# Optimization experiments

Hardware: AMD Instinct MI355X
Metric: run time of the kernel (lower is better)

## Reference

```python
import jax, jax.numpy as jnp
import numpy as np

B, C, H, W = 16, 512, 32, 32
CI = C // 2
EPS = 1e-5


def _lin_params(k, din, dout):
    kw, kb = jax.random.split(k)
    w = jax.random.normal(kw, (dout, din), jnp.float32) * (1.0 / np.sqrt(din))
    b = jax.random.normal(kb, (dout,), jnp.float32) * 0.01
    return w, b


def _bn_params(k):
    k1, k2, k3, k4 = jax.random.split(k, 4)
    g = 1.0 + 0.05 * jax.random.normal(k1, (C,), jnp.float32)
    b = 0.05 * jax.random.normal(k2, (C,), jnp.float32)
    m = 0.1 * jax.random.normal(k3, (C,), jnp.float32)
    v = jax.random.uniform(k4, (C,), jnp.float32, 0.5, 1.5)
    return g, b, m, v


def setup_inputs() -> dict:
    key = jax.random.key(0)
    ks = jax.random.split(key, 12)
    inp = {
        'rgb_cm': jax.random.normal(ks[0], (B, C, H, W), jnp.float32),
        'flow_cm': jax.random.normal(ks[1], (B, C, H, W), jnp.float32),
    }
    for i, pfx in enumerate(['1', '2']):
        g, b, m, v = _bn_params(ks[2 + 5 * i])
        inp[f'bn{pfx}_g'], inp[f'bn{pfx}_b'] = g, b
        inp[f'bn{pfx}_m'], inp[f'bn{pfx}_v'] = m, v
        inp[f'th{pfx}_w'], inp[f'th{pfx}_b'] = _lin_params(ks[3 + 5 * i], C, CI)
        inp[f'ph{pfx}_w'], inp[f'ph{pfx}_b'] = _lin_params(ks[4 + 5 * i], C, CI)
        inp[f'g{pfx}_w'], inp[f'g{pfx}_b'] = _lin_params(ks[5 + 5 * i], C, CI)
        inp[f'w{pfx}_w'], inp[f'w{pfx}_b'] = _lin_params(ks[6 + 5 * i], CI, C)
    return inp


def _bn_relu(x, g, b, m, v):
    # x: [B, C, num]; eval-mode BatchNorm1d over channel dim, then ReLU
    scale = (g * jax.lax.rsqrt(v + EPS))[None, :, None]
    shift = (b - m * g * jax.lax.rsqrt(v + EPS))[None, :, None]
    return jax.nn.relu(x * scale + shift)


def _can(A, Bx, bn_g, bn_b, bn_m, bn_v, th_w, th_b, ph_w, ph_b, g_w, g_b, w_w, w_b):
    # A, Bx: [B, C, num]
    A = _bn_relu(A, bn_g, bn_b, bn_m, bn_v).transpose(0, 2, 1)   # [B, num, C]
    Bx = _bn_relu(Bx, bn_g, bn_b, bn_m, bn_v).transpose(0, 2, 1)  # [B, num, C]
    x_theta = A @ th_w.T + th_b      # [B, num, CI]
    x_phi = Bx @ ph_w.T + ph_b       # [B, num, CI]
    attn = jnp.einsum('bnc,bmc->bnm', x_theta, x_phi)  # [B, num, num] (unscaled)
    f_div_C = jax.nn.softmax(attn, axis=-1)
    g_x = A @ g_w.T + g_b            # [B, num, CI]
    y = jnp.einsum('bnm,bmc->bnc', f_div_C, g_x)
    W_y = y @ w_w.T + w_b            # [B, num, C]
    return (A + W_y).transpose(0, 2, 1)  # [B, C, num]


def reference(rgb_cm, flow_cm,
              bn1_g, bn1_b, bn1_m, bn1_v, th1_w, th1_b, ph1_w, ph1_b, g1_w, g1_b, w1_w, w1_b,
              bn2_g, bn2_b, bn2_m, bn2_v, th2_w, th2_b, ph2_w, ph2_b, g2_w, g2_b, w2_w, w2_b):
    b, c, h, w = rgb_cm.shape
    rgb_f = rgb_cm.reshape(b, c, h * w)
    flow_f = flow_cm.reshape(b, c, h * w)
    att_rgb = _can(rgb_f, flow_f, bn1_g, bn1_b, bn1_m, bn1_v,
                   th1_w, th1_b, ph1_w, ph1_b, g1_w, g1_b, w1_w, w1_b)
    att_flow = _can(flow_f, rgb_f, bn2_g, bn2_b, bn2_m, bn2_v,
                    th2_w, th2_b, ph2_w, ph2_b, g2_w, g2_b, w2_w, w2_b)
    return att_rgb.reshape(b, c, h, w), att_flow.reshape(b, c, h, w)
```

## Files before the change

kernel.cpp:

```cpp
#include <hip/hip_runtime.h>


typedef __bf16 bf16x8 __attribute__((ext_vector_type(8)));
typedef float  f32x4  __attribute__((ext_vector_type(4)));
typedef float  f32x16 __attribute__((ext_vector_type(16)));
typedef unsigned u32x4 __attribute__((ext_vector_type(4)));
static_assert(sizeof(bf16x8) == 16, "bf16x8 must be 16B");

constexpr int KTILE = 8704;
constexpr int VTILE = 10240;
constexpr int KINST = 32 * KTILE;
constexpr int VINST = 32 * VTILE;

__device__ __forceinline__ ushort f2bf(float x) {
  unsigned u = __builtin_bit_cast(unsigned, x);
  u = (u + 0x7fffu + ((u >> 16) & 1u)) >> 16;
  return (ushort)u;
}
__device__ __forceinline__ unsigned packbf(float lo, float hi) {
  return (unsigned)f2bf(lo) | ((unsigned)f2bf(hi) << 16);
}
__device__ __forceinline__ void gload_lds16(const ushort* g, ushort* l) {
  __builtin_amdgcn_global_load_lds(
      (const __attribute__((address_space(1))) void*)g,
      (__attribute__((address_space(3))) void*)l, 16, 0, 0);
}

struct WcvtArgs { const float* src[8]; };
__global__ __launch_bounds__(256) void wcvt8_k(WcvtArgs a, ushort* __restrict__ dst) {
  const int which = blockIdx.y;
  const int i = blockIdx.x * 256 + threadIdx.x;
  dst[(size_t)which * 131072 + i] = f2bf(a.src[which][i]);
}

__global__ __launch_bounds__(256) void bn2_k(
    const float* __restrict__ rgb, const float* __restrict__ flow,
    const float* __restrict__ g1, const float* __restrict__ b1,
    const float* __restrict__ m1, const float* __restrict__ v1,
    const float* __restrict__ g2, const float* __restrict__ b2,
    const float* __restrict__ m2, const float* __restrict__ v2,
    ushort* __restrict__ Abn1, ushort* __restrict__ Bbn1,
    ushort* __restrict__ Abn2, ushort* __restrict__ Bbn2)
{
  const int z = blockIdx.z;
  const int b = z >> 1, which = z & 1;
  const float* src = which ? flow : rgb;
  ushort* o1 = which ? Bbn1 : Abn1;
  ushort* o2 = which ? Abn2 : Bbn2;
  src += (size_t)b * 512 * 1024;
  o1  += (size_t)b * 1024 * 512;
  o2  += (size_t)b * 1024 * 512;

  __shared__ float tile[32][33];
  const int n0 = blockIdx.x * 32, c0 = blockIdx.y * 32;
  const int tx = threadIdx.x & 31, ty = threadIdx.x >> 5;

  #pragma unroll
  for (int i = 0; i < 4; ++i) {
    const int c = c0 + ty + i * 8;
    tile[ty + i * 8][tx] = src[(size_t)c * 1024 + n0 + tx];
  }
  __syncthreads();
  const int c = c0 + tx;
  const float s1 = g1[c] * rsqrtf(v1[c] + 1e-5f);
  const float h1 = b1[c] - m1[c] * s1;
  const float s2 = g2[c] * rsqrtf(v2[c] + 1e-5f);
  const float h2 = b2[c] - m2[c] * s2;
  #pragma unroll
  for (int i = 0; i < 4; ++i) {
    const int n = n0 + ty + i * 8;
    const float x = tile[tx][ty + i * 8];
    o1[(size_t)n * 512 + c] = f2bf(fmaxf(x * s1 + h1, 0.f));
    o2[(size_t)n * 512 + c] = f2bf(fmaxf(x * s2 + h2, 0.f));
  }
}

struct ProjDesc { const ushort* W; const ushort* act; const float* bias;
                  ushort* out; int mode; };
struct ProjArgs { ProjDesc d[6]; };

__global__ __launch_bounds__(256, 2) void proj128_k(ProjArgs pa) {
  __shared__ __align__(16) ushort Al[128 * 80];
  __shared__ __align__(16) ushort Bl[128 * 80];

  const int bx = blockIdx.x;
  const int mb = bx >> 3, nb = bx & 7;
  const int by = blockIdx.y;
  const ProjDesc d = pa.d[by >> 4];
  const int inst = by & 15;
  const ushort* A = d.W;
  const ushort* Bact = d.act + (size_t)inst * 524288;

  const int tid = threadIdx.x;
  const int w = tid >> 6, lane = tid & 63;
  const int q = lane >> 4, lm = lane & 15;
  const int m0 = mb * 128, n0 = nb * 128;

  int row[4], c8[4];
  #pragma unroll
  for (int i = 0; i < 4; ++i) { int g = i * 256 + tid; row[i] = g >> 3; c8[i] = g & 7; }

  bf16x8 ast[4], bst[4];
  auto sload = [&](int kk) {
    #pragma unroll
    for (int i = 0; i < 4; ++i) {
      ast[i] = *reinterpret_cast<const bf16x8*>(A + (size_t)(m0 + row[i]) * 512 + kk + c8[i] * 8);
      bst[i] = *reinterpret_cast<const bf16x8*>(Bact + (size_t)(n0 + row[i]) * 512 + kk + c8[i] * 8);
    }
  };
  sload(0);

  f32x4 acc[4][4];
  #pragma unroll
  for (int i = 0; i < 4; ++i)
    #pragma unroll
    for (int j = 0; j < 4; ++j) acc[i][j] = (f32x4){0.f, 0.f, 0.f, 0.f};

  const int wm = (w >> 1) * 64, wn = (w & 1) * 64;

  for (int t = 0; t < 8; ++t) {
    __syncthreads();
    #pragma unroll
    for (int i = 0; i < 4; ++i) {
      *reinterpret_cast<bf16x8*>(Al + row[i] * 80 + c8[i] * 8) = ast[i];
      *reinterpret_cast<bf16x8*>(Bl + row[i] * 80 + c8[i] * 8) = bst[i];
    }
    __syncthreads();
    if (t < 7) sload((t + 1) * 64);
    #pragma unroll
    for (int ks = 0; ks < 2; ++ks) {
      bf16x8 af[4], bfr[4];
      #pragma unroll
      for (int f = 0; f < 4; ++f)
        af[f] = *reinterpret_cast<const bf16x8*>(Al + (wm + f * 16 + lm) * 80 + ks * 32 + q * 8);
      #pragma unroll
      for (int f = 0; f < 4; ++f)
        bfr[f] = *reinterpret_cast<const bf16x8*>(Bl + (wn + f * 16 + lm) * 80 + ks * 32 + q * 8);
      __builtin_amdgcn_s_setprio(1);
      #pragma unroll
      for (int fi = 0; fi < 4; ++fi)
        #pragma unroll
        for (int fj = 0; fj < 4; ++fj)
          acc[fi][fj] = __builtin_amdgcn_mfma_f32_16x16x32_bf16(af[fi], bfr[fj], acc[fi][fj], 0, 0, 0);
      __builtin_amdgcn_s_setprio(0);
    }
  }

  if (d.mode == 0) {
    ushort* out = d.out + (size_t)inst * 262144;
    #pragma unroll
    for (int fi = 0; fi < 4; ++fi)
      #pragma unroll
      for (int fj = 0; fj < 4; ++fj) {
        const int m4 = m0 + wm + fi * 16 + q * 4;
        const int n  = n0 + wn + fj * 16 + lm;
        float4 bi = *reinterpret_cast<const float4*>(d.bias + m4);
        ushort4 u = {f2bf(acc[fi][fj][0] + bi.x), f2bf(acc[fi][fj][1] + bi.y),
                     f2bf(acc[fi][fj][2] + bi.z), f2bf(acc[fi][fj][3] + bi.w)};
        *reinterpret_cast<ushort4*>(out + (size_t)n * 256 + m4) = u;
      }
  } else if (d.mode == 1) {
    ushort* out = d.out + (size_t)inst * KINST;
    #pragma unroll
    for (int fi = 0; fi < 4; ++fi)
      #pragma unroll
      for (int fj = 0; fj < 4; ++fj) {
        const int m4 = m0 + wm + fi * 16 + q * 4;
        const int n  = n0 + wn + fj * 16 + lm;
        float4 bi = *reinterpret_cast<const float4*>(d.bias + m4);
        ushort4 u = {f2bf(acc[fi][fj][0] + bi.x), f2bf(acc[fi][fj][1] + bi.y),
                     f2bf(acc[fi][fj][2] + bi.z), f2bf(acc[fi][fj][3] + bi.w)};
        *reinterpret_cast<ushort4*>(out + (size_t)(n >> 5) * KTILE + (n & 31) * 264 + m4) = u;
      }
  } else {
    ushort* out = d.out + (size_t)inst * VINST;
    #pragma unroll
    for (int fi = 0; fi < 4; ++fi)
      #pragma unroll
      for (int fj = 0; fj < 4; ++fj) {
        const int n = n0 + wn + fj * 16 + lm;
        const size_t base = (size_t)(n >> 5) * VTILE + ((n & 31) >> 3) * 8 + (n & 7);
        #pragma unroll
        for (int j = 0; j < 4; ++j) {
          const int m = m0 + wm + fi * 16 + q * 4 + j;
          out[base + (size_t)m * 40] = f2bf(acc[fi][fj][j] + d.bias[m]);
        }
      }
  }
}

__global__ __launch_bounds__(256, 2) void flash_k(
    const ushort* __restrict__ Qp, const ushort* __restrict__ Kg,
    const ushort* __restrict__ Vg, ushort* __restrict__ Op)
{
  __shared__ __align__(16) ushort KV[2][KTILE + VTILE];
  __shared__ float2 stat2[2][32];

  const int raw = blockIdx.x;
  const int xcd = raw & 7, loc = raw >> 3;
  const int inst = xcd * 4 + (loc >> 4);
  const int qb = loc & 15;

  const int tid = threadIdx.x;
  const int w = tid >> 6, lane = tid & 63;
  const int u = w & 1, p = w >> 1;
  const int h = lane >> 5, lm5 = lane & 31;

  const ushort* Q  = Qp + (size_t)inst * 262144;
  const ushort* Kt = Kg + (size_t)inst * KINST + (size_t)p * 16 * KTILE;
  const ushort* Vt = Vg + (size_t)inst * VINST + (size_t)p * 16 * VTILE;

  ushort* Klds = &KV[p][0];
  ushort* Vlds = &KV[p][KTILE];

  const int nrow0 = qb * 64 + u * 32;

  bf16x8 qf[16];
  #pragma unroll
  for (int cs = 0; cs < 16; ++cs)
    qf[cs] = *reinterpret_cast<const bf16x8*>(
        Q + (size_t)(nrow0 + lm5) * 256 + cs * 16 + h * 8);

  f32x16 acc[8];
  #pragma unroll
  for (int cb = 0; cb < 8; ++cb)
    #pragma unroll
    for (int i = 0; i < 16; ++i) acc[cb][i] = 0.f;

  float run_m = -__builtin_inff();
  float run_l = 0.f;

  auto stageK = [&](int t) {
    const ushort* src = Kt + (size_t)t * KTILE;
    const int base = u ? 9 : 0;
    #pragma unroll
    for (int j = 0; j < 9; ++j)
      if (u == 0 || j < 8)
        gload_lds16(src + (base + j) * 512 + lane * 8, Klds + (base + j) * 512);
  };
  auto stageV = [&](int t) {
    const ushort* src = Vt + (size_t)t * VTILE;
    #pragma unroll
    for (int j = 0; j < 10; ++j)
      gload_lds16(src + (u * 10 + j) * 512 + lane * 8, Vlds + (u * 10 + j) * 512);
  };

  stageK(0);
  stageV(0);
  asm volatile("s_waitcnt vmcnt(0)" ::: "memory");
  __builtin_amdgcn_sched_barrier(0);
  __builtin_amdgcn_s_barrier();

  for (int t = 0; t < 16; ++t) {
    f32x16 S;
    #pragma unroll
    for (int i = 0; i < 16; ++i) S[i] = 0.f;
    #pragma unroll
    for (int cs = 0; cs < 16; ++cs) {
      bf16x8 kf = *reinterpret_cast<const bf16x8*>(
          Klds + lm5 * 264 + (cs * 2 + h) * 8);
      S = __builtin_amdgcn_mfma_f32_32x32x16_bf16(kf, qf[cs], S, 0, 0, 0);
    }

    __builtin_amdgcn_sched_barrier(0);
    asm volatile("s_waitcnt vmcnt(0)" ::: "memory");
    __builtin_amdgcn_sched_barrier(0);
    __builtin_amdgcn_s_barrier();
    __builtin_amdgcn_sched_barrier(0);
    if (t < 15) stageK(t + 1);

    float ml = fmaxf(fmaxf(fmaxf(S[0], S[1]), fmaxf(S[2], S[3])),
                     fmaxf(fmaxf(S[4], S[5]), fmaxf(S[6], S[7])));
    ml = fmaxf(ml, fmaxf(fmaxf(fmaxf(S[8], S[9]), fmaxf(S[10], S[11])),
                         fmaxf(fmaxf(S[12], S[13]), fmaxf(S[14], S[15]))));
    ml = fmaxf(ml, __shfl_xor(ml, 32));
    const float mnew = fmaxf(run_m, ml);
    if (!__all(ml <= run_m + 8.f)) {
      const float sc = __expf(run_m - mnew);
      run_m = mnew;
      run_l *= sc;
      #pragma unroll
      for (int cb = 0; cb < 8; ++cb) acc[cb] *= sc;
    }
    #pragma unroll
    for (int i = 0; i < 16; ++i) S[i] = __expf(S[i] - run_m);
    float ts = ((S[0] + S[1]) + (S[2] + S[3])) + ((S[4] + S[5]) + (S[6] + S[7]));
    ts += ((S[8] + S[9]) + (S[10] + S[11])) + ((S[12] + S[13]) + (S[14] + S[15]));
    ts += __shfl_xor(ts, 32);
    run_l += ts;

    const unsigned pk0 = packbf(S[0], S[1]),   pk1 = packbf(S[2], S[3]);
    const unsigned pk2 = packbf(S[4], S[5]),   pk3 = packbf(S[6], S[7]);
    const unsigned pk4 = packbf(S[8], S[9]),   pk5 = packbf(S[10], S[11]);
    const unsigned pk6 = packbf(S[12], S[13]), pk7 = packbf(S[14], S[15]);
    const unsigned sx0 = __shfl_xor(pk0, 32), sx1 = __shfl_xor(pk1, 32);
    const unsigned sx2 = __shfl_xor(pk2, 32), sx3 = __shfl_xor(pk3, 32);
    const unsigned sx4 = __shfl_xor(pk4, 32), sx5 = __shfl_xor(pk5, 32);
    const unsigned sx6 = __shfl_xor(pk6, 32), sx7 = __shfl_xor(pk7, 32);
    const bool hh = (h != 0);
    u32x4 B0, B1;
    B0[0] = hh ? sx2 : pk0;  B0[1] = hh ? sx3 : pk1;
    B0[2] = hh ? pk2 : sx0;  B0[3] = hh ? pk3 : sx1;
    B1[0] = hh ? sx6 : pk4;  B1[1] = hh ? sx7 : pk5;
    B1[2] = hh ? pk6 : sx4;  B1[3] = hh ? pk7 : sx5;
    const bf16x8 pf0 = __builtin_bit_cast(bf16x8, B0);
    const bf16x8 pf1 = __builtin_bit_cast(bf16x8, B1);

    #pragma unroll
    for (int cb = 0; cb < 8; ++cb) {
      bf16x8 v0 = *reinterpret_cast<const bf16x8*>(
          Vlds + (cb * 32 + lm5) * 40 + h * 8);
      bf16x8 v1 = *reinterpret_cast<const bf16x8*>(
          Vlds + (cb * 32 + lm5) * 40 + (2 + h) * 8);
      acc[cb] = __builtin_amdgcn_mfma_f32_32x32x16_bf16(v0, pf0, acc[cb], 0, 0, 0);
      acc[cb] = __builtin_amdgcn_mfma_f32_32x32x16_bf16(v1, pf1, acc[cb], 0, 0, 0);
    }

    __builtin_amdgcn_sched_barrier(0);
    __builtin_amdgcn_s_barrier();
    __builtin_amdgcn_sched_barrier(0);
    if (t < 15) {
      stageV(t + 1);
      asm volatile("s_waitcnt vmcnt(10)" ::: "memory");
    } else {
      asm volatile("s_waitcnt vmcnt(0)" ::: "memory");
    }
    __builtin_amdgcn_sched_barrier(0);
    __builtin_amdgcn_s_barrier();
    __builtin_amdgcn_sched_barrier(0);
  }

  __syncthreads();
  if (p == 1 && lane < 32) stat2[u][lm5] = make_float2(run_m, run_l);

  float a0 = 1.f, a1 = 0.f, inv = 1.f;
  float4* mb = reinterpret_cast<float4*>(&KV[0][0]);
  #pragma unroll
  for (int half = 0; half < 2; ++half) {
    __syncthreads();
    if (p == 1) {
      #pragma unroll
      for (int cb2 = 0; cb2 < 4; ++cb2) {
        const int cb = half * 4 + cb2;
        #pragma unroll
        for (int r4 = 0; r4 < 4; ++r4) {
          float4 v = {acc[cb][r4 * 4 + 0], acc[cb][r4 * 4 + 1],
                      acc[cb][r4 * 4 + 2], acc[cb][r4 * 4 + 3]};
          mb[u * 1024 + cb2 * 256 + r4 * 64 + lane] = v;
        }
      }
    }
    __syncthreads();
    if (p == 0) {
      if (half == 0) {
        const float2 s1 = stat2[u][lm5];
        const float M = fmaxf(run_m, s1.x);
        a0 = __expf(run_m - M);
        a1 = __expf(s1.x - M);
        inv = 1.f / (a0 * run_l + a1 * s1.y);
      }
      ushort* Ob = Op + (size_t)inst * 262144 + (size_t)(nrow0 + lm5) * 256;
      #pragma unroll
      for (int cb2 = 0; cb2 < 4; ++cb2) {
        const int cb = half * 4 + cb2;
        #pragma unroll
        for (int r4 = 0; r4 < 4; ++r4) {
          float4 o = mb[u * 1024 + cb2 * 256 + r4 * 64 + lane];
          ushort4 s;
          s.x = f2bf((a0 * acc[cb][r4 * 4 + 0] + a1 * o.x) * inv);
          s.y = f2bf((a0 * acc[cb][r4 * 4 + 1] + a1 * o.y) * inv);
          s.z = f2bf((a0 * acc[cb][r4 * 4 + 2] + a1 * o.z) * inv);
          s.w = f2bf((a0 * acc[cb][r4 * 4 + 3] + a1 * o.w) * inv);
          *reinterpret_cast<ushort4*>(Ob + cb * 32 + r4 * 8 + h * 4) = s;
        }
      }
    }
  }
}

struct WgemmArgs {
  const ushort* yb[2]; const ushort* wW[2]; const float* wb[2];
  const float* src[2]; const float* g[2]; const float* bb[2];
  const float* mm[2]; const float* vv[2];
};

__global__ __launch_bounds__(256, 2) void wgemm_epi_k(WgemmArgs a, float* __restrict__ outp) {
  __shared__ __align__(16) ushort Al[128 * 80];
  __shared__ __align__(16) ushort Bl[128 * 80];

  const int bx = blockIdx.x;
  const int mb = bx >> 2, nb = bx & 3;
  const int by = blockIdx.y;
  const int mod = by >> 4, b = by & 15;

  const ushort* A  = a.yb[mod] + (size_t)b * 262144;
  const ushort* Bw = a.wW[mod];
  const float* wb  = a.wb[mod];
  const float* src = a.src[mod] + (size_t)b * 512 * 1024;
  const float* g   = a.g[mod];
  const float* bbp = a.bb[mod];
  const float* mm  = a.mm[mod];
  const float* vv  = a.vv[mod];
  float* out = outp + (size_t)mod * 16 * 512 * 1024 + (size_t)b * 512 * 1024;

  const int tid = threadIdx.x;
  const int w = tid >> 6, lane = tid & 63;
  const int q = lane >> 4, lm = lane & 15;
  const int m0 = mb * 128, n0 = nb * 128;

  int row[4], c8[4];
  #pragma unroll
  for (int i = 0; i < 4; ++i) { int gg = i * 256 + tid; row[i] = gg >> 3; c8[i] = gg & 7; }

  bf16x8 ast[4], bst[4];
  auto sload = [&](int kk) {
    #pragma unroll
    for (int i = 0; i < 4; ++i) {
      ast[i] = *reinterpret_cast<const bf16x8*>(A  + (size_t)(m0 + row[i]) * 256 + kk + c8[i] * 8);
      bst[i] = *reinterpret_cast<const bf16x8*>(Bw + (size_t)(n0 + row[i]) * 256 + kk + c8[i] * 8);
    }
  };
  sload(0);

  f32x4 acc[4][4];
  #pragma unroll
  for (int i = 0; i < 4; ++i)
    #pragma unroll
    for (int j = 0; j < 4; ++j) acc[i][j] = (f32x4){0.f, 0.f, 0.f, 0.f};

  const int wm = (w >> 1) * 64, wn = (w & 1) * 64;

  for (int t = 0; t < 4; ++t) {
    __syncthreads();
    #pragma unroll
    for (int i = 0; i < 4; ++i) {
      *reinterpret_cast<bf16x8*>(Al + row[i] * 80 + c8[i] * 8) = ast[i];
      *reinterpret_cast<bf16x8*>(Bl + row[i] * 80 + c8[i] * 8) = bst[i];
    }
    __syncthreads();
    if (t < 3) sload((t + 1) * 64);
    #pragma unroll
    for (int ks = 0; ks < 2; ++ks) {
      bf16x8 af[4], bfr[4];
      #pragma unroll
      for (int f = 0; f < 4; ++f)
        af[f] = *reinterpret_cast<const bf16x8*>(Al + (wm + f * 16 + lm) * 80 + ks * 32 + q * 8);
      #pragma unroll
      for (int f = 0; f < 4; ++f)
        bfr[f] = *reinterpret_cast<const bf16x8*>(Bl + (wn + f * 16 + lm) * 80 + ks * 32 + q * 8);
      __builtin_amdgcn_s_setprio(1);
      #pragma unroll
      for (int fi = 0; fi < 4; ++fi)
        #pragma unroll
        for (int fj = 0; fj < 4; ++fj)
          acc[fi][fj] = __builtin_amdgcn_mfma_f32_16x16x32_bf16(af[fi], bfr[fj], acc[fi][fj], 0, 0, 0);
      __builtin_amdgcn_s_setprio(0);
    }
  }

  #pragma unroll
  for (int fj = 0; fj < 4; ++fj) {
    const int c = n0 + wn + fj * 16 + lm;
    const float sc = g[c] * rsqrtf(vv[c] + 1e-5f);
    const float sh = bbp[c] - mm[c] * sc;
    const float bv = wb[c];
    #pragma unroll
    for (int fi = 0; fi < 4; ++fi) {
      const int n4 = m0 + wm + fi * 16 + q * 4;
      const size_t base = (size_t)c * 1024 + n4;
      float4 x = *reinterpret_cast<const float4*>(src + base);
      float4 v;
      v.x = acc[fi][fj][0] + bv + fmaxf(x.x * sc + sh, 0.f);
      v.y = acc[fi][fj][1] + bv + fmaxf(x.y * sc + sh, 0.f);
      v.z = acc[fi][fj][2] + bv + fmaxf(x.z * sc + sh, 0.f);
      v.w = acc[fi][fj][3] + bv + fmaxf(x.w * sc + sh, 0.f);
      *reinterpret_cast<float4*>(out + base) = v;
    }
  }
}

constexpr size_t MB = 1ull << 20;
constexpr size_t OFF_WBF = 0;
constexpr size_t OFF_BN  = 2 * MB;
constexpr size_t OFF_TH  = 66 * MB;
constexpr size_t OFF_KG  = 82 * MB;
constexpr size_t OFF_VG  = 100 * MB;
constexpr size_t OFF_YB  = 120 * MB;

extern "C" void kernel_launch(void* const* d_in, const int* in_sizes, int n_in,
                              void* d_out, int out_size, void* d_ws, size_t ws_size,
                              hipStream_t stream) {
  const float* rgb  = (const float*)d_in[0];
  const float* flow = (const float*)d_in[1];
  auto in = [&](int mod, int j) { return (const float*)d_in[2 + mod * 12 + j]; };

  char* ws = (char*)d_ws;
  ushort* wbf  = (ushort*)(ws + OFF_WBF);
  ushort* Abn1 = (ushort*)(ws + OFF_BN);
  ushort* Bbn1 = (ushort*)(ws + OFF_BN + 16 * MB);
  ushort* Abn2 = (ushort*)(ws + OFF_BN + 32 * MB);
  ushort* Bbn2 = (ushort*)(ws + OFF_BN + 48 * MB);
  ushort* th   = (ushort*)(ws + OFF_TH);
  ushort* Kgx  = (ushort*)(ws + OFF_KG);
  ushort* Vgx  = (ushort*)(ws + OFF_VG);
  ushort* yb   = (ushort*)(ws + OFF_YB);
  float*  out  = (float*)d_out;

  const size_t MODSTR = (size_t)16 * 262144;

  WcvtArgs wa;
  for (int mod = 0; mod < 2; ++mod) {
    wa.src[mod * 4 + 0] = in(mod, 4);
    wa.src[mod * 4 + 1] = in(mod, 6);
    wa.src[mod * 4 + 2] = in(mod, 8);
    wa.src[mod * 4 + 3] = in(mod, 10);
  }
  wcvt8_k<<<dim3(512, 8), 256, 0, stream>>>(wa, wbf);

  bn2_k<<<dim3(32, 16, 32), 256, 0, stream>>>(
      rgb, flow,
      in(0, 0), in(0, 1), in(0, 2), in(0, 3),
      in(1, 0), in(1, 1), in(1, 2), in(1, 3),
      Abn1, Bbn1, Abn2, Bbn2);

  ProjArgs pa;
  for (int mod = 0; mod < 2; ++mod) {
    const ushort* wb4 = wbf + (size_t)mod * 4 * 131072;
    ushort* Abn = mod ? Abn2 : Abn1;
    ushort* Bbn = mod ? Bbn2 : Bbn1;
    pa.d[mod * 3 + 0] = {wb4,              Abn, in(mod, 5), th + mod * MODSTR,               0};
    pa.d[mod * 3 + 1] = {wb4 + 131072,     Bbn, in(mod, 7), Kgx + (size_t)mod * 16 * KINST, 1};
    pa.d[mod * 3 + 2] = {wb4 + 2 * 131072, Abn, in(mod, 9), Vgx + (size_t)mod * 16 * VINST, 2};
  }
  proj128_k<<<dim3(16, 96), 256, 0, stream>>>(pa);

  flash_k<<<dim3(512), 256, 0, stream>>>(th, Kgx, Vgx, yb);

  WgemmArgs ga;
  for (int mod = 0; mod < 2; ++mod) {
    ga.yb[mod]  = yb + mod * MODSTR;
    ga.wW[mod]  = wbf + (size_t)(mod * 4 + 3) * 131072;
    ga.wb[mod]  = in(mod, 11);
    ga.src[mod] = mod ? flow : rgb;
    ga.g[mod]   = in(mod, 0);
    ga.bb[mod]  = in(mod, 1);
    ga.mm[mod]  = in(mod, 2);
    ga.vv[mod]  = in(mod, 3);
  }
  wgemm_epi_k<<<dim3(32, 32), 256, 0, stream>>>(ga, out);
}
```

Before: 171.8 us.

## Vectorize weight conversion and BN transpose, split attention MFMA accumulator chain

The weight-conversion kernel now handles four floats per thread with float4 loads and ushort4 stores, and its grid shrinks to match. The BN+ReLU transpose kernel applies both BN variants before the transpose, packs the two bf16 results into one shared-memory word, and writes 8-byte vectorized outputs in place of scalar 2-byte stores. The QK^T loop in the attention kernel splits its 16 dependent MFMAs into two independent accumulator chains summed at the end, to hide MFMA latency. This costs extra accumulator registers and changes the floating-point summation order.

```diff
diff --git a/kernel.cpp b/kernel.cpp
--- a/kernel.cpp
+++ b/kernel.cpp
@@ -29,8 +29,10 @@
 struct WcvtArgs { const float* src[8]; };
 __global__ __launch_bounds__(256) void wcvt8_k(WcvtArgs a, ushort* __restrict__ dst) {
   const int which = blockIdx.y;
-  const int i = blockIdx.x * 256 + threadIdx.x;
-  dst[(size_t)which * 131072 + i] = f2bf(a.src[which][i]);
+  const int i = (blockIdx.x * 256 + threadIdx.x) * 4;
+  float4 x = *reinterpret_cast<const float4*>(a.src[which] + i);
+  ushort4 u = {f2bf(x.x), f2bf(x.y), f2bf(x.z), f2bf(x.w)};
+  *reinterpret_cast<ushort4*>(dst + (size_t)which * 131072 + i) = u;
 }
 
 __global__ __launch_bounds__(256) void bn2_k(
@@ -51,28 +53,40 @@
   o1  += (size_t)b * 1024 * 512;
   o2  += (size_t)b * 1024 * 512;
 
-  __shared__ float tile[32][33];
+  __shared__ unsigned tileU[32][36];
   const int n0 = blockIdx.x * 32, c0 = blockIdx.y * 32;
-  const int tx = threadIdx.x & 31, ty = threadIdx.x >> 5;
-
-  #pragma unroll
-  for (int i = 0; i < 4; ++i) {
-    const int c = c0 + ty + i * 8;
-    tile[ty + i * 8][tx] = src[(size_t)c * 1024 + n0 + tx];
+
+  const int rc = threadIdx.x >> 3, nq = threadIdx.x & 7;
+  {
+    const int c = c0 + rc;
+    const float s1 = g1[c] * rsqrtf(v1[c] + 1e-5f);
+    const float h1 = b1[c] - m1[c] * s1;
+    const float s2 = g2[c] * rsqrtf(v2[c] + 1e-5f);
+    const float h2 = b2[c] - m2[c] * s2;
+    float4 x = *reinterpret_cast<const float4*>(src + (size_t)c * 1024 + n0 + nq * 4);
+    u32x4 u;
+    u[0] = packbf(fmaxf(x.x * s1 + h1, 0.f), fmaxf(x.x * s2 + h2, 0.f));
+    u[1] = packbf(fmaxf(x.y * s1 + h1, 0.f), fmaxf(x.y * s2 + h2, 0.f));
+    u[2] = packbf(fmaxf(x.z * s1 + h1, 0.f), fmaxf(x.z * s2 + h2, 0.f));
+    u[3] = packbf(fmaxf(x.w * s1 + h1, 0.f), fmaxf(x.w * s2 + h2, 0.f));
+    *reinterpret_cast<u32x4*>(&tileU[rc][nq * 4]) = u;
   }
   __syncthreads();
-  const int c = c0 + tx;
-  const float s1 = g1[c] * rsqrtf(v1[c] + 1e-5f);
-  const float h1 = b1[c] - m1[c] * s1;
-  const float s2 = g2[c] * rsqrtf(v2[c] + 1e-5f);
-  const float h2 = b2[c] - m2[c] * s2;
-  #pragma unroll
-  for (int i = 0; i < 4; ++i) {
-    const int n = n0 + ty + i * 8;
-    const float x = tile[tx][ty + i * 8];
-    o1[(size_t)n * 512 + c] = f2bf(fmaxf(x * s1 + h1, 0.f));
-    o2[(size_t)n * 512 + c] = f2bf(fmaxf(x * s2 + h2, 0.f));
-  }
+  const int r = threadIdx.x >> 3, cq = threadIdx.x & 7;
+  ushort4 w1, w2;
+  {
+    const unsigned u0 = tileU[cq * 4 + 0][r];
+    const unsigned u1 = tileU[cq * 4 + 1][r];
+    const unsigned u2 = tileU[cq * 4 + 2][r];
+    const unsigned u3 = tileU[cq * 4 + 3][r];
+    w1 = (ushort4){(ushort)(u0 & 0xffff), (ushort)(u1 & 0xffff),
+                   (ushort)(u2 & 0xffff), (ushort)(u3 & 0xffff)};
+    w2 = (ushort4){(ushort)(u0 >> 16), (ushort)(u1 >> 16),
+                   (ushort)(u2 >> 16), (ushort)(u3 >> 16)};
+  }
+  const size_t base = (size_t)(n0 + r) * 512 + c0 + cq * 4;
+  *reinterpret_cast<ushort4*>(o1 + base) = w1;
+  *reinterpret_cast<ushort4*>(o2 + base) = w2;
 }
 
 struct ProjDesc { const ushort* W; const ushort* act; const float* bias;
@@ -252,15 +266,19 @@
   __builtin_amdgcn_s_barrier();
 
   for (int t = 0; t < 16; ++t) {
-    f32x16 S;
-    #pragma unroll
-    for (int i = 0; i < 16; ++i) S[i] = 0.f;
-    #pragma unroll
-    for (int cs = 0; cs < 16; ++cs) {
-      bf16x8 kf = *reinterpret_cast<const bf16x8*>(
+    f32x16 Sa, Sb;
+    #pragma unroll
+    for (int i = 0; i < 16; ++i) { Sa[i] = 0.f; Sb[i] = 0.f; }
+    #pragma unroll
+    for (int cs = 0; cs < 8; ++cs) {
+      bf16x8 kfa = *reinterpret_cast<const bf16x8*>(
           Klds + lm5 * 264 + (cs * 2 + h) * 8);
-      S = __builtin_amdgcn_mfma_f32_32x32x16_bf16(kf, qf[cs], S, 0, 0, 0);
-    }
+      bf16x8 kfb = *reinterpret_cast<const bf16x8*>(
+          Klds + lm5 * 264 + ((cs + 8) * 2 + h) * 8);
+      Sa = __builtin_amdgcn_mfma_f32_32x32x16_bf16(kfa, qf[cs], Sa, 0, 0, 0);
+      Sb = __builtin_amdgcn_mfma_f32_32x32x16_bf16(kfb, qf[cs + 8], Sb, 0, 0, 0);
+    }
+    f32x16 S = Sa + Sb;
 
     __builtin_amdgcn_sched_barrier(0);
     asm volatile("s_waitcnt vmcnt(0)" ::: "memory");
@@ -515,7 +533,7 @@
     wa.src[mod * 4 + 2] = in(mod, 8);
     wa.src[mod * 4 + 3] = in(mod, 10);
   }
-  wcvt8_k<<<dim3(512, 8), 256, 0, stream>>>(wa, wbf);
+  wcvt8_k<<<dim3(128, 8), 256, 0, stream>>>(wa, wbf);
 
   bn2_k<<<dim3(32, 16, 32), 256, 0, stream>>>(
       rgb, flow,
```

Result: slower. 211.7 us (+23.2%).
